# Kernel tuning notes

Hardware: AMD Instinct MI355X
Metric: run time of the kernel (lower is better)

The kernel has to match this reference:

```python
import jax, jax.numpy as jnp
import numpy as np

N, E, D = 50000, 800000, 128
H, C = 8, 16  # heads, hidden_per_head; H*C == D
NEG_SLOPE = 0.15


def setup_inputs() -> dict:
    key = jax.random.key(0)
    ks = jax.random.split(key, 8)
    x = jax.random.normal(ks[0], (N, D), dtype=jnp.float32)
    edge_index = jax.random.randint(ks[1], (2, E), 0, N, dtype=jnp.int32)
    s = 1.0 / np.sqrt(D)
    return {
        "x": x,
        "edge_index": edge_index,
        "ln_g": jnp.ones((D,), jnp.float32),
        "ln_b": jnp.zeros((D,), jnp.float32),
        "W_l": jax.random.normal(ks[2], (D, H * C), jnp.float32) * s,
        "b_l": jnp.zeros((H * C,), jnp.float32),
        "W_r": jax.random.normal(ks[3], (D, H * C), jnp.float32) * s,
        "b_r": jnp.zeros((H * C,), jnp.float32),
        "att": jax.random.normal(ks[4], (H, C), jnp.float32) * (1.0 / np.sqrt(C)),
        "bias": jnp.zeros((H * C,), jnp.float32),
    }


def _layernorm(x, g, b, eps=1e-5):
    mu = jnp.mean(x, axis=-1, keepdims=True)
    var = jnp.mean(jnp.square(x - mu), axis=-1, keepdims=True)
    return (x - mu) * jax.lax.rsqrt(var + eps) * g + b


def reference(x, edge_index, ln_g, ln_b, W_l, b_l, W_r, b_r, att, bias):
    src, dst = edge_index[0], edge_index[1]
    h = _layernorm(x, ln_g, ln_b)                      # [N, D]
    xl = (h @ W_l + b_l).reshape(N, H, C)              # source-side transform
    xr = (h @ W_r + b_r).reshape(N, H, C)              # target-side transform
    # GATv2 edge attention: leaky_relu(x_j + x_i) . att
    e = xl[src] + xr[dst]                              # [E, H, C]
    e_act = jnp.where(e > 0, e, NEG_SLOPE * e)
    alpha = jnp.einsum('ehc,hc->eh', e_act, att)       # [E, H]
    # segment softmax over edges grouped by destination node
    m = jax.ops.segment_max(alpha, dst, num_segments=N)   # [N, H]
    ex = jnp.exp(alpha - m[dst])                           # [E, H]
    denom = jax.ops.segment_sum(ex, dst, num_segments=N)  # [N, H]
    a = ex / (denom[dst] + 1e-16)                          # [E, H]
    # weighted message aggregation (scatter-add)
    msg = xl[src] * a[:, :, None]                          # [E, H, C]
    out = jax.ops.segment_sum(msg, dst, num_segments=N)   # [N, H, C]
    out = out.reshape(N, H * C) + bias
    h2 = jax.nn.relu(out)                                  # act='relu', dropout off (eval)
    return x + h2                                          # proj is Identity (in_dim == out_dim)
```

## Files before the change

kernel.cpp:

```cpp
#include <hip/hip_runtime.h>

typedef unsigned int uint32;
typedef __attribute__((ext_vector_type(4))) float f32x4;
typedef __attribute__((ext_vector_type(2))) float f32x2;
typedef __attribute__((ext_vector_type(8))) short bf16x8;

#define NEG_SLOPE 0.15f
#define GPB 2

__device__ __forceinline__ float2 bf2_to_f2(uint32 u) {
  union { uint32 i; float f; } a, b;
  a.i = u << 16;
  b.i = u & 0xffff0000u;
  return make_float2(a.f, b.f);
}

__device__ __forceinline__ f32x2 unpk(uint32 u) {
  union { uint32 i; float f; } lo, hi;
  lo.i = u << 16; hi.i = u & 0xffff0000u;
  f32x2 r; r.x = lo.f; r.y = hi.f; return r;
}

__device__ __forceinline__ f32x2 vmax2(f32x2 a, f32x2 b) {
  f32x2 r; r.x = fmaxf(a.x, b.x); r.y = fmaxf(a.y, b.y); return r;
}

__device__ __forceinline__ float bf_to_f(unsigned short s) {
  union { uint32 i; float f; } u;
  u.i = ((uint32)s) << 16;
  return u.f;
}

__device__ __forceinline__ unsigned short f32_to_bf16(float f) {
  union { float f; uint32 i; } u; u.f = f;
  uint32 r = u.i + 0x7fffu + ((u.i >> 16) & 1u);
  return (unsigned short)(r >> 16);
}

__device__ __forceinline__ uint32 pack_bf2(float x, float y) {
  return (uint32)f32_to_bf16(x) | ((uint32)f32_to_bf16(y) << 16);
}

__device__ __forceinline__ float2 loadpair(const void* p, size_t i, int isbf) {
  if (isbf) return bf2_to_f2(((const uint32*)p)[i]);
  return ((const float2*)p)[i];
}

__device__ __forceinline__ float loadelem(const void* p, size_t i, int isbf) {
  if (isbf) return bf_to_f(((const unsigned short*)p)[i]);
  return ((const float*)p)[i];
}

__device__ __forceinline__ int get_isbf(const void* ln_g) {
  return ((const uint32*)ln_g)[0] != 0x3F800000u ? 1 : 0;
}

__global__ __launch_bounds__(256) void prep_hist_k(
    const void* __restrict__ Wl, const void* __restrict__ Wr,
    const void* __restrict__ bl, const void* __restrict__ br,
    const void* __restrict__ att, const void* __restrict__ obias,
    const void* __restrict__ ln_g, const void* __restrict__ ln_b,
    unsigned short* __restrict__ Wt, float* __restrict__ c1,
    float* __restrict__ c2b, float* __restrict__ att_c,
    float* __restrict__ obias_c,
    const int* __restrict__ ei, int* __restrict__ cntg,
    int E, int Eb, int R)
{
  int b = blockIdx.x;
  if (b < 128) {
    int isbf = get_isbf(ln_g);
    int id = b * 256 + threadIdx.x;
    int n = id >> 7, k = id & 127;
    float g = loadelem(ln_g, k, isbf);
    float v = (n < 128) ? loadelem(Wl, (size_t)k * 128 + n, isbf)
                        : loadelem(Wr, (size_t)k * 128 + (n - 128), isbf);
    Wt[(size_t)n * 128 + k] = f32_to_bf16(g * v);
    if (id < 128) {
      att_c[id]   = loadelem(att, id, isbf);
      obias_c[id] = loadelem(obias, id, isbf);
    }
  } else if (b < 192) {
    int isbf = get_isbf(ln_g);
    int w = threadIdx.x >> 6, lane = threadIdx.x & 63;
    int n = (b - 128) * 4 + w;
    const void* W = (n < 128) ? Wl : Wr;
    int nn = n & 127;
    float s1 = 0.f, s2 = 0.f;
    #pragma unroll
    for (int t = 0; t < 2; ++t) {
      int kk = t * 64 + lane;
      float wv = loadelem(W, (size_t)kk * 128 + nn, isbf);
      s1 += loadelem(ln_g, kk, isbf) * wv;
      s2 += loadelem(ln_b, kk, isbf) * wv;
    }
    #pragma unroll
    for (int off = 1; off < 64; off <<= 1) {
      s1 += __shfl_xor(s1, off, 64);
      s2 += __shfl_xor(s2, off, 64);
    }
    if (lane == 0) {
      c1[n] = s1;
      c2b[n] = s2 + ((n < 128) ? loadelem(bl, nn, isbf) : loadelem(br, nn, isbf));
    }
  } else {
    __shared__ int hist[256];
    int hb = b - 192, tid = threadIdx.x;
    hist[tid] = 0;
    __syncthreads();
    int startE = hb * Eb, endE = min(E, startE + Eb);
    const int* dp = ei + E;
    int nfull = (endE > startE) ? ((endE - startE) >> 2) : 0;
    for (int g = tid; g < nfull; g += 256) {
      int4 d = *(const int4*)(dp + startE + g * 4);
      atomicAdd(&hist[((uint32)d.x) >> 8], 1);
      atomicAdd(&hist[((uint32)d.y) >> 8], 1);
      atomicAdd(&hist[((uint32)d.z) >> 8], 1);
      atomicAdd(&hist[((uint32)d.w) >> 8], 1);
    }
    int rem0 = startE + nfull * 4;
    if (rem0 + tid < endE) atomicAdd(&hist[((uint32)dp[rem0 + tid]) >> 8], 1);
    __syncthreads();
    if (tid < R) cntg[tid * 256 + hb] = hist[tid];
  }
}

__global__ __launch_bounds__(1024) void scanA_k(const int* __restrict__ in,
    int* __restrict__ outl, int* __restrict__ psum, int n)
{
  __shared__ int wsum[16];
  int tid = threadIdx.x, lane = tid & 63, w = tid >> 6;
  int i = blockIdx.x * 1024 + tid;
  int v = (i < n) ? in[i] : 0;
  int xs = v;
  #pragma unroll
  for (int off = 1; off < 64; off <<= 1) {
    int y = __shfl_up(xs, off, 64);
    if (lane >= off) xs += y;
  }
  if (lane == 63) wsum[w] = xs;
  __syncthreads();
  if (w == 0) {
    int sv = (lane < 16) ? wsum[lane] : 0;
    int ss = sv;
    #pragma unroll
    for (int off = 1; off < 16; off <<= 1) {
      int y = __shfl_up(ss, off, 64);
      if (lane >= off) ss += y;
    }
    if (lane < 16) wsum[lane] = ss - sv;
    if (lane == 15) psum[blockIdx.x] = ss;
  }
  __syncthreads();
  if (i < n) outl[i] = wsum[w] + xs - v;
}

__global__ void scanB_k(int* __restrict__ psum, int* __restrict__ total, int nb) {
  int lane = threadIdx.x;
  int v = (lane < nb) ? psum[lane] : 0;
  int xs = v;
  #pragma unroll
  for (int off = 1; off < 64; off <<= 1) {
    int y = __shfl_up(xs, off, 64);
    if (lane >= off) xs += y;
  }
  if (lane < nb) psum[lane] = xs - v;
  if (lane == 63) *total = xs;
}

__device__ __forceinline__ void load_group(bf16x8* slot, const void* x,
                                           int isbf, int rl, int quad) {
  if (isbf) {
    const unsigned short* xp = (const unsigned short*)x + (size_t)rl * 128 + quad * 8;
    #pragma unroll
    for (int kc = 0; kc < 4; ++kc) slot[kc] = *(const bf16x8*)(xp + kc * 32);
  } else {
    const float* xp = (const float*)x + (size_t)rl * 128 + quad * 8;
    #pragma unroll
    for (int kc = 0; kc < 4; ++kc) {
      float4 a0 = *(const float4*)(xp + kc * 32);
      float4 a1 = *(const float4*)(xp + kc * 32 + 4);
      union { bf16x8 v; uint32 u[4]; } av;
      av.u[0] = pack_bf2(a0.x, a0.y);
      av.u[1] = pack_bf2(a0.z, a0.w);
      av.u[2] = pack_bf2(a1.x, a1.y);
      av.u[3] = pack_bf2(a1.z, a1.w);
      slot[kc] = av.v;
    }
  }
}

__global__ __launch_bounds__(256) void bin_gemm_k(
    const int* __restrict__ ei, const int* __restrict__ cbase,
    const int* __restrict__ psum, uint32* __restrict__ binned,
    int E, int Eb, int R,
    const void* __restrict__ x, const void* __restrict__ ln_g,
    const unsigned short* __restrict__ Wt,
    const float* __restrict__ c1, const float* __restrict__ c2b,
    unsigned short* __restrict__ xl, unsigned short* __restrict__ xr,
    int nrows)
{
  if (blockIdx.x < 256) {
    __shared__ int cur[256];
    int b = blockIdx.x, tid = threadIdx.x;
    if (tid < R) {
      int idx = tid * 256 + b;
      cur[tid] = cbase[idx] + psum[idx >> 10];
    }
    __syncthreads();
    int startE = b * Eb, endE = min(E, startE + Eb);
    int nfull = (endE > startE) ? ((endE - startE) >> 2) : 0;
    for (int g = tid; g < nfull; g += 256) {
      int e = startE + g * 4;
      int4 s = *(const int4*)(ei + e);
      int4 d = *(const int4*)(ei + E + e);
      int p0 = atomicAdd(&cur[((uint32)d.x) >> 8], 1);
      binned[p0] = (uint32)s.x | (((uint32)d.x & 255u) << 16);
      int p1 = atomicAdd(&cur[((uint32)d.y) >> 8], 1);
      binned[p1] = (uint32)s.y | (((uint32)d.y & 255u) << 16);
      int p2 = atomicAdd(&cur[((uint32)d.z) >> 8], 1);
      binned[p2] = (uint32)s.z | (((uint32)d.z & 255u) << 16);
      int p3 = atomicAdd(&cur[((uint32)d.w) >> 8], 1);
      binned[p3] = (uint32)s.w | (((uint32)d.w & 255u) << 16);
    }
    int rem0 = startE + nfull * 4;
    if (rem0 + tid < endE) {
      int e = rem0 + tid;
      uint32 src = (uint32)ei[e], dst = (uint32)ei[E + e];
      int pos = atomicAdd(&cur[dst >> 8], 1);
      binned[pos] = src | ((dst & 255u) << 16);
    }
    return;
  }

  int bid  = blockIdx.x - 256;
  int isbf = get_isbf(ln_g);
  int lane = threadIdx.x & 63;
  int w    = threadIdx.x >> 6;
  int m16  = lane & 15;
  int quad = lane >> 4;
  int base = bid * (GPB * 16);

  bf16x8 araw[GPB][4];
  #pragma unroll
  for (int g2 = 0; g2 < GPB; ++g2) {
    int r = base + g2 * 16 + m16;
    if (r >= nrows) r = nrows - 1;
    load_group(araw[g2], x, isbf, r, quad);
  }

  bf16x8 bfrag[4][4];
  #pragma unroll
  for (int nt = 0; nt < 4; ++nt)
    #pragma unroll
    for (int kc = 0; kc < 4; ++kc)
      bfrag[nt][kc] = *(const bf16x8*)(
          Wt + (size_t)(w * 64 + nt * 16 + m16) * 128 + kc * 32 + quad * 8);

  float c1v[4], c2v[4];
  #pragma unroll
  for (int nt = 0; nt < 4; ++nt) {
    int col = w * 64 + nt * 16 + m16;
    c1v[nt] = c1[col];
    c2v[nt] = c2b[col];
  }

  unsigned short* dst = (w < 2) ? xl : xr;
  int cb = (w & 1) * 64;

  #pragma unroll
  for (int g2 = 0; g2 < GPB; ++g2) {
    bf16x8* A = araw[g2];

    float s = 0.f, s2 = 0.f;
    #pragma unroll
    for (int kc = 0; kc < 4; ++kc) {
      union { bf16x8 v; uint32 u[4]; } uu; uu.v = A[kc];
      #pragma unroll
      for (int j = 0; j < 4; ++j) {
        float2 t = bf2_to_f2(uu.u[j]);
        s += t.x + t.y;
        s2 += t.x * t.x + t.y * t.y;
      }
    }
    s  += __shfl_xor(s, 16, 64);  s2 += __shfl_xor(s2, 16, 64);
    s  += __shfl_xor(s, 32, 64);  s2 += __shfl_xor(s2, 32, 64);
    float mu  = s * (1.0f / 128.0f);
    float var = fmaxf(s2 * (1.0f / 128.0f) - mu * mu, 0.0f);
    float rs  = rsqrtf(var + 1e-5f);
    float rm  = rs * mu;

    f32x4 acc[4];
    #pragma unroll
    for (int nt = 0; nt < 4; ++nt) acc[nt] = (f32x4){0.f, 0.f, 0.f, 0.f};
    #pragma unroll
    for (int kc = 0; kc < 4; ++kc)
      #pragma unroll
      for (int nt = 0; nt < 4; ++nt)
        acc[nt] = __builtin_amdgcn_mfma_f32_16x16x32_bf16(A[kc], bfrag[nt][kc], acc[nt], 0, 0, 0);

    float rs_j[4], rm_j[4];
    #pragma unroll
    for (int j = 0; j < 4; ++j) {
      rs_j[j] = __shfl(rs, quad * 4 + j, 64);
      rm_j[j] = __shfl(rm, quad * 4 + j, 64);
    }

    #pragma unroll
    for (int nt = 0; nt < 4; ++nt) {
      #pragma unroll
      for (int j = 0; j < 4; ++j) {
        int r = base + g2 * 16 + quad * 4 + j;
        if (r < nrows)
          dst[(size_t)r * 128 + cb + nt * 16 + m16] =
              f32_to_bf16(rs_j[j] * acc[nt][j] - rm_j[j] * c1v[nt] + c2v[nt]);
      }
    }
  }
}

__global__ __launch_bounds__(256) void rangesort_k(
    const uint32* __restrict__ binned, const int* __restrict__ cbase,
    const int* __restrict__ psum,
    int* __restrict__ starts, unsigned short* __restrict__ csr16,
    int E, int N, int R)
{
  __shared__ int hist[256];
  __shared__ int wsum[4];
  __shared__ int cur[256];
  int r = blockIdx.x;
  int tid = threadIdx.x, lane = tid & 63, w = tid >> 6;
  int i0 = r * 256;
  int segStart = cbase[i0] + psum[i0 >> 10];
  int segEnd;
  if (r + 1 < R) {
    int i1 = (r + 1) * 256;
    segEnd = cbase[i1] + psum[i1 >> 10];
  } else {
    segEnd = E;
  }

  hist[tid] = 0;
  __syncthreads();
  for (int i = segStart + tid; i < segEnd; i += 256)
    atomicAdd(&hist[(binned[i] >> 16) & 255u], 1);
  __syncthreads();

  int v = hist[tid];
  int xs = v;
  #pragma unroll
  for (int off = 1; off < 64; off <<= 1) {
    int y = __shfl_up(xs, off, 64);
    if (lane >= off) xs += y;
  }
  if (lane == 63) wsum[w] = xs;
  __syncthreads();
  int woff = 0;
  #pragma unroll
  for (int i = 0; i < 4; ++i) if (i < w) woff += wsum[i];
  int st = segStart + woff + xs - v;
  int node = (r << 8) + tid;
  if (node < N) starts[node] = st;
  cur[tid] = st;
  __syncthreads();

  for (int i = segStart + tid; i < segEnd; i += 256) {
    uint32 pk = binned[i];
    int d = (pk >> 16) & 255u;
    int pos = atomicAdd(&cur[d], 1);
    csr16[pos] = (unsigned short)(pk & 0xffffu);
  }
}

__global__ __launch_bounds__(256) void agg_k(
    const uint32* __restrict__ xl32,
    const uint32* __restrict__ xr32,
    const int* __restrict__ starts, const unsigned short* __restrict__ csr16,
    const void* __restrict__ x, const void* __restrict__ ln_g,
    const float* __restrict__ att_c, const float* __restrict__ obias_c,
    void* __restrict__ out, int n)
{
  int node = blockIdx.x * 4 + (threadIdx.x >> 6);
  if (node >= n) return;
  int isbf = get_isbf(ln_g);
  int lane = threadIdx.x & 63;
  int q    = lane >> 4;
  int sub  = lane & 15;

  uint4 xru = *(const uint4*)(xr32 + (size_t)node * 64 + sub * 4);
  f32x2 xr0 = unpk(xru.x), xr1 = unpk(xru.y), xr2 = unpk(xru.z), xr3 = unpk(xru.w);
  const f32x2* atp = (const f32x2*)(att_c + sub * 8);
  f32x2 t0 = atp[0], t1 = atp[1], t2 = atp[2], t3 = atp[3];
  f32x2 ns; ns.x = NEG_SLOPE; ns.y = NEG_SLOPE;

  float lsum = 0.f;
  f32x2 ac[4];
  #pragma unroll
  for (int i = 0; i < 4; ++i) { ac[i].x = 0.f; ac[i].y = 0.f; }

  int p0 = starts[node], p1 = starts[node + 1];
  if (p0 < p1) {
    int pmax = p1 - 1;
    bool v0 = (p0 + q) < p1;
    bool v1 = (p0 + 4 + q) < p1;
    uint4 xu  = *(const uint4*)(xl32 + (size_t)csr16[min(p0 + q, pmax)] * 64 + sub * 4);
    uint4 xu1 = *(const uint4*)(xl32 + (size_t)csr16[min(p0 + 4 + q, pmax)] * 64 + sub * 4);

    for (int p = p0; p < p1; p += 4) {
      int pe2 = p + 8 + q;
      uint4 xu2 = *(const uint4*)(xl32 + (size_t)csr16[min(pe2, pmax)] * 64 + sub * 4);

      f32x2 a0 = unpk(xu.x), a1 = unpk(xu.y), a2 = unpk(xu.z), a3 = unpk(xu.w);
      f32x2 e0 = a0 + xr0, e1 = a1 + xr1, e2 = a2 + xr2, e3 = a3 + xr3;
      e0 = vmax2(e0, e0 * ns);
      e1 = vmax2(e1, e1 * ns);
      e2 = vmax2(e2, e2 * ns);
      e3 = vmax2(e3, e3 * ns);
      f32x2 dt = e0 * t0;
      dt += e1 * t1;
      dt += e2 * t2;
      dt += e3 * t3;
      float dot = dt.x + dt.y;
      dot += __shfl_xor(dot, 1, 64);
      float pw = v0 ? __expf(dot) : 0.f;
      lsum += pw;
      f32x2 pw2; pw2.x = pw; pw2.y = pw;
      ac[0] += pw2 * a0;
      ac[1] += pw2 * a1;
      ac[2] += pw2 * a2;
      ac[3] += pw2 * a3;

      xu = xu1; xu1 = xu2;
      v0 = v1; v1 = pe2 < p1;
    }
  }

  lsum += __shfl_xor(lsum, 16, 64);
  lsum += __shfl_xor(lsum, 32, 64);
  #pragma unroll
  for (int i = 0; i < 4; ++i) {
    ac[i].x += __shfl_xor(ac[i].x, 16, 64);
    ac[i].x += __shfl_xor(ac[i].x, 32, 64);
    ac[i].y += __shfl_xor(ac[i].y, 16, 64);
    ac[i].y += __shfl_xor(ac[i].y, 32, 64);
  }

  if (q == 0) {
    float inv = 1.0f / (lsum + 1e-16f);
    float4 b0 = *(const float4*)(obias_c + sub * 8);
    float4 b1 = *(const float4*)(obias_c + sub * 8 + 4);
    float2 rx[4];
    #pragma unroll
    for (int i = 0; i < 4; ++i)
      rx[i] = loadpair(x, (size_t)node * 64 + sub * 4 + i, isbf);
    float o0 = rx[0].x + fmaxf(ac[0].x * inv + b0.x, 0.f);
    float o1 = rx[0].y + fmaxf(ac[0].y * inv + b0.y, 0.f);
    float o2 = rx[1].x + fmaxf(ac[1].x * inv + b0.z, 0.f);
    float o3 = rx[1].y + fmaxf(ac[1].y * inv + b0.w, 0.f);
    float o4 = rx[2].x + fmaxf(ac[2].x * inv + b1.x, 0.f);
    float o5 = rx[2].y + fmaxf(ac[2].y * inv + b1.y, 0.f);
    float o6 = rx[3].x + fmaxf(ac[3].x * inv + b1.z, 0.f);
    float o7 = rx[3].y + fmaxf(ac[3].y * inv + b1.w, 0.f);
    if (isbf) {
      uint4 ov;
      ov.x = pack_bf2(o0, o1); ov.y = pack_bf2(o2, o3);
      ov.z = pack_bf2(o4, o5); ov.w = pack_bf2(o6, o7);
      *(uint4*)((uint32*)out + (size_t)node * 64 + sub * 4) = ov;
    } else {
      float4 f0 = make_float4(o0, o1, o2, o3);
      float4 f1 = make_float4(o4, o5, o6, o7);
      *(float4*)((float*)out + (size_t)node * 128 + sub * 8) = f0;
      *(float4*)((float*)out + (size_t)node * 128 + sub * 8 + 4) = f1;
    }
  }
}

static inline char* align16(char* p) {
  return (char*)(((uintptr_t)p + 15) & ~(uintptr_t)15);
}

extern "C" void kernel_launch(void* const* d_in, const int* in_sizes, int n_in,
                              void* d_out, int out_size, void* d_ws, size_t ws_size,
                              hipStream_t stream) {
  const void* x    = d_in[0];
  const int*  ei   = (const int*)d_in[1];
  const void* ln_g = d_in[2];
  const void* ln_b = d_in[3];
  const void* Wl   = d_in[4];
  const void* bl   = d_in[5];
  const void* Wr   = d_in[6];
  const void* br   = d_in[7];
  const void* att  = d_in[8];
  const void* bias = d_in[9];

  int N = in_sizes[0] / 128;
  int E = in_sizes[1] / 2;
  int R = (N + 255) >> 8;
  int L = R * 256;
  int Eb = (((E + 255) / 256) + 3) & ~3;

  char* ws = (char*)d_ws;
  unsigned short* xl = (unsigned short*)ws; ws = align16(ws + (size_t)N * 128 * 2);
  unsigned short* xr = (unsigned short*)ws; ws = align16(ws + (size_t)N * 128 * 2);
  unsigned short* Wt = (unsigned short*)ws; ws = align16(ws + 256 * 128 * 2);
  float* c1      = (float*)ws;              ws = align16(ws + 256 * 4);
  float* c2b     = (float*)ws;              ws = align16(ws + 256 * 4);
  float* att_c   = (float*)ws;              ws = align16(ws + 128 * 4);
  float* obias_c = (float*)ws;              ws = align16(ws + 128 * 4);
  int* cntg      = (int*)ws;                ws = align16(ws + (size_t)L * 4);
  int* cbase     = (int*)ws;                ws = align16(ws + (size_t)L * 4);
  int* psum      = (int*)ws;                ws = align16(ws + 64 * 4);
  int* starts    = (int*)ws;                ws = align16(ws + (size_t)(N + 1) * 4);
  uint32* binned = (uint32*)ws;             ws = align16(ws + (size_t)E * 4);
  unsigned short* csr16 = (unsigned short*)ws; ws = align16(ws + (size_t)E * 2);

  int nbScan = (L + 1023) / 1024;
  int nGemmB = (N + GPB * 16 - 1) / (GPB * 16);

  hipLaunchKernelGGL(prep_hist_k, dim3(448), dim3(256), 0, stream,
                     Wl, Wr, bl, br, att, bias, ln_g, ln_b,
                     Wt, c1, c2b, att_c, obias_c,
                     ei, cntg, E, Eb, R);
  hipLaunchKernelGGL(scanA_k, dim3(nbScan), dim3(1024), 0, stream, cntg, cbase, psum, L);
  hipLaunchKernelGGL(scanB_k, dim3(1), dim3(64), 0, stream, psum, starts + N, nbScan);
  hipLaunchKernelGGL(bin_gemm_k, dim3(256 + nGemmB), dim3(256), 0, stream,
                     ei, cbase, psum, binned, E, Eb, R,
                     x, ln_g, Wt, c1, c2b, xl, xr, N);
  hipLaunchKernelGGL(rangesort_k, dim3(R), dim3(256), 0, stream,
                     binned, cbase, psum, starts, csr16, E, N, R);
  hipLaunchKernelGGL(agg_k, dim3((N + 3) / 4), dim3(256), 0, stream,
                     (const uint32*)xl, (const uint32*)xr, starts, csr16,
                     x, ln_g, att_c, obias_c, d_out, N);
}
```

Before: 184.6 us.

## Fold block-sum scan into consumers, widen rangesort blocks, deepen agg prefetch

Removes the separate single-block scanB kernel. Each bin_gemm and rangesort block now recomputes the small prefix over psum in shared memory, and rangesort writes the total starts[N]. rangesort blocks grow from 256 to 1024 threads so each 256-node range is histogrammed and scattered with more parallelism. agg_k deepens its software pipeline to three row loads in flight and prefetches csr indices further ahead, aiming to hide gather latency at the cost of more registers.

```diff
diff --git a/kernel.cpp b/kernel.cpp
--- a/kernel.cpp
+++ b/kernel.cpp
@@ -154,19 +154,6 @@
   if (i < n) outl[i] = wsum[w] + xs - v;
 }
 
-__global__ void scanB_k(int* __restrict__ psum, int* __restrict__ total, int nb) {
-  int lane = threadIdx.x;
-  int v = (lane < nb) ? psum[lane] : 0;
-  int xs = v;
-  #pragma unroll
-  for (int off = 1; off < 64; off <<= 1) {
-    int y = __shfl_up(xs, off, 64);
-    if (lane >= off) xs += y;
-  }
-  if (lane < nb) psum[lane] = xs - v;
-  if (lane == 63) *total = xs;
-}
-
 __device__ __forceinline__ void load_group(bf16x8* slot, const void* x,
                                            int isbf, int rl, int quad) {
   if (isbf) {
@@ -192,7 +179,7 @@
 __global__ __launch_bounds__(256) void bin_gemm_k(
     const int* __restrict__ ei, const int* __restrict__ cbase,
     const int* __restrict__ psum, uint32* __restrict__ binned,
-    int E, int Eb, int R,
+    int E, int Eb, int R, int nbScan,
     const void* __restrict__ x, const void* __restrict__ ln_g,
     const unsigned short* __restrict__ Wt,
     const float* __restrict__ c1, const float* __restrict__ c2b,
@@ -201,10 +188,22 @@
 {
   if (blockIdx.x < 256) {
     __shared__ int cur[256];
+    __shared__ int spsum[64];
     int b = blockIdx.x, tid = threadIdx.x;
+    if (tid < 64) {
+      int v = (tid < nbScan) ? psum[tid] : 0;
+      int xs = v;
+      #pragma unroll
+      for (int off = 1; off < 64; off <<= 1) {
+        int y = __shfl_up(xs, off, 64);
+        if (tid >= off) xs += y;
+      }
+      spsum[tid] = xs - v;
+    }
+    __syncthreads();
     if (tid < R) {
       int idx = tid * 256 + b;
-      cur[tid] = cbase[idx] + psum[idx >> 10];
+      cur[tid] = cbase[idx] + spsum[idx >> 10];
     }
     __syncthreads();
     int startE = b * Eb, endE = min(E, startE + Eb);
@@ -318,52 +317,71 @@
   }
 }
 
-__global__ __launch_bounds__(256) void rangesort_k(
+__global__ __launch_bounds__(1024) void rangesort_k(
     const uint32* __restrict__ binned, const int* __restrict__ cbase,
     const int* __restrict__ psum,
     int* __restrict__ starts, unsigned short* __restrict__ csr16,
-    int E, int N, int R)
+    int E, int N, int R, int nbScan)
 {
   __shared__ int hist[256];
   __shared__ int wsum[4];
   __shared__ int cur[256];
+  __shared__ int spsum[64];
   int r = blockIdx.x;
   int tid = threadIdx.x, lane = tid & 63, w = tid >> 6;
+
+  if (tid < 64) {
+    int pv = (tid < nbScan) ? psum[tid] : 0;
+    int pxs = pv;
+    #pragma unroll
+    for (int off = 1; off < 64; off <<= 1) {
+      int y = __shfl_up(pxs, off, 64);
+      if (tid >= off) pxs += y;
+    }
+    spsum[tid] = pxs - pv;
+  }
+  if (tid < 256) hist[tid] = 0;
+  __syncthreads();
+
   int i0 = r * 256;
-  int segStart = cbase[i0] + psum[i0 >> 10];
+  int segStart = cbase[i0] + spsum[i0 >> 10];
   int segEnd;
   if (r + 1 < R) {
     int i1 = (r + 1) * 256;
-    segEnd = cbase[i1] + psum[i1 >> 10];
+    segEnd = cbase[i1] + spsum[i1 >> 10];
   } else {
     segEnd = E;
   }
-
-  hist[tid] = 0;
-  __syncthreads();
-  for (int i = segStart + tid; i < segEnd; i += 256)
+  if (r == 0 && tid == 0) starts[N] = E;
+
+  for (int i = segStart + tid; i < segEnd; i += 1024)
     atomicAdd(&hist[(binned[i] >> 16) & 255u], 1);
   __syncthreads();
 
-  int v = hist[tid];
-  int xs = v;
-  #pragma unroll
-  for (int off = 1; off < 64; off <<= 1) {
-    int y = __shfl_up(xs, off, 64);
-    if (lane >= off) xs += y;
-  }
-  if (lane == 63) wsum[w] = xs;
+  int v = 0, xs = 0;
+  if (tid < 256) {
+    v = hist[tid];
+    xs = v;
+    #pragma unroll
+    for (int off = 1; off < 64; off <<= 1) {
+      int y = __shfl_up(xs, off, 64);
+      if (lane >= off) xs += y;
+    }
+    if (lane == 63) wsum[w] = xs;
+  }
   __syncthreads();
-  int woff = 0;
-  #pragma unroll
-  for (int i = 0; i < 4; ++i) if (i < w) woff += wsum[i];
-  int st = segStart + woff + xs - v;
-  int node = (r << 8) + tid;
-  if (node < N) starts[node] = st;
-  cur[tid] = st;
+  if (tid < 256) {
+    int woff = 0;
+    #pragma unroll
+    for (int i = 0; i < 4; ++i) if (i < w) woff += wsum[i];
+    int st = segStart + woff + xs - v;
+    int node = (r << 8) + tid;
+    if (node < N) starts[node] = st;
+    cur[tid] = st;
+  }
   __syncthreads();
 
-  for (int i = segStart + tid; i < segEnd; i += 256) {
+  for (int i = segStart + tid; i < segEnd; i += 1024) {
     uint32 pk = binned[i];
     int d = (pk >> 16) & 255u;
     int pos = atomicAdd(&cur[d], 1);
@@ -400,14 +418,20 @@
   int p0 = starts[node], p1 = starts[node + 1];
   if (p0 < p1) {
     int pmax = p1 - 1;
-    bool v0 = (p0 + q) < p1;
-    bool v1 = (p0 + 4 + q) < p1;
-    uint4 xu  = *(const uint4*)(xl32 + (size_t)csr16[min(p0 + q, pmax)] * 64 + sub * 4);
-    uint4 xu1 = *(const uint4*)(xl32 + (size_t)csr16[min(p0 + 4 + q, pmax)] * 64 + sub * 4);
+    int bq = p0 + q;
+    uint32 so = (uint32)(sub * 4);
+    uint32 j0 = csr16[min(bq,      pmax)];
+    uint32 j1 = csr16[min(bq + 4,  pmax)];
+    uint32 j2 = csr16[min(bq + 8,  pmax)];
+    uint32 j3 = csr16[min(bq + 12, pmax)];
+    uint32 j4 = csr16[min(bq + 16, pmax)];
+    uint4 xu  = *(const uint4*)(xl32 + (j0 * 64u + so));
+    uint4 xu1 = *(const uint4*)(xl32 + (j1 * 64u + so));
+    uint4 xu2 = *(const uint4*)(xl32 + (j2 * 64u + so));
 
     for (int p = p0; p < p1; p += 4) {
-      int pe2 = p + 8 + q;
-      uint4 xu2 = *(const uint4*)(xl32 + (size_t)csr16[min(pe2, pmax)] * 64 + sub * 4);
+      uint32 j5 = csr16[min(p + 20 + q, pmax)];
+      uint4 xu3 = *(const uint4*)(xl32 + (j3 * 64u + so));
 
       f32x2 a0 = unpk(xu.x), a1 = unpk(xu.y), a2 = unpk(xu.z), a3 = unpk(xu.w);
       f32x2 e0 = a0 + xr0, e1 = a1 + xr1, e2 = a2 + xr2, e3 = a3 + xr3;
@@ -421,7 +445,7 @@
       dt += e3 * t3;
       float dot = dt.x + dt.y;
       dot += __shfl_xor(dot, 1, 64);
-      float pw = v0 ? __expf(dot) : 0.f;
+      float pw = ((p + q) < p1) ? __expf(dot) : 0.f;
       lsum += pw;
       f32x2 pw2; pw2.x = pw; pw2.y = pw;
       ac[0] += pw2 * a0;
@@ -429,8 +453,8 @@
       ac[2] += pw2 * a2;
       ac[3] += pw2 * a3;
 
-      xu = xu1; xu1 = xu2;
-      v0 = v1; v1 = pe2 < p1;
+      xu = xu1; xu1 = xu2; xu2 = xu3;
+      j3 = j4; j4 = j5;
     }
   }
 
@@ -521,12 +545,11 @@
                      Wt, c1, c2b, att_c, obias_c,
                      ei, cntg, E, Eb, R);
   hipLaunchKernelGGL(scanA_k, dim3(nbScan), dim3(1024), 0, stream, cntg, cbase, psum, L);
-  hipLaunchKernelGGL(scanB_k, dim3(1), dim3(64), 0, stream, psum, starts + N, nbScan);
   hipLaunchKernelGGL(bin_gemm_k, dim3(256 + nGemmB), dim3(256), 0, stream,
-                     ei, cbase, psum, binned, E, Eb, R,
+                     ei, cbase, psum, binned, E, Eb, R, nbScan,
                      x, ln_g, Wt, c1, c2b, xl, xr, N);
-  hipLaunchKernelGGL(rangesort_k, dim3(R), dim3(256), 0, stream,
-                     binned, cbase, psum, starts, csr16, E, N, R);
+  hipLaunchKernelGGL(rangesort_k, dim3(R), dim3(1024), 0, stream,
+                     binned, cbase, psum, starts, csr16, E, N, R, nbScan);
   hipLaunchKernelGGL(agg_k, dim3((N + 3) / 4), dim3(256), 0, stream,
                      (const uint32*)xl, (const uint32*)xr, starts, csr16,
                      x, ln_g, att_c, obias_c, d_out, N);
```

After: 178.5 us. 3.3% less time.
